# Optimization experiments

Measured on AMD Instinct MI355X. Metric: run time of the kernel, lower is better.

The kernel has to match this reference:

```python
import jax, jax.numpy as jnp
import numpy as np


def reference(x, phi, sigma, M_phi_plus, M_phi_minus, M_u, padded_sl):
    """STU forward: spectral FFT convolution + autoregressive input term.

    x:   (B, L, D) input sequence
    phi: (L, K) time-domain spectral filters (top-K Hankel eigenvectors);
         V = rfft(phi, n=padded_sl) matches the module's precomputed V.
    sigma: (K,) Hankel eigenvalues
    M_phi_plus/minus: (K, D, D) per-filter projections
    M_u: (k_u, D, D) AR-on-input matrices
    """
    B, L, D = x.shape
    K = sigma.shape[0]
    n = padded_sl  # FFT length for causal linear convolution

    # Alternating-sign trick for the 'minus' featurization:
    # sum_j (-1)^j phi_j u_{t-j} = (-1)^t * conv(phi, sgn*u)_t
    sgn = jnp.where(jnp.arange(L) % 2 == 0, 1.0, -1.0).astype(x.dtype)[None, :, None]  # (1,L,1)

    V = jnp.fft.rfft(phi, n=n, axis=0)                       # (n//2+1, K) complex
    U = jnp.fft.rfft(jnp.stack([x, x * sgn], axis=-1), n=n, axis=1)  # (B, n//2+1, D, 2)
    prod = V[None, :, :, None, None] * U[:, :, None, :, :]    # (B, n//2+1, K, D, 2)
    conv = jnp.fft.irfft(prod, n=n, axis=1)[:, :L]            # (B, L, K, D, 2) causal conv
    U_plus = conv[..., 0]
    U_minus = conv[..., 1] * sgn[..., None]                   # undo sign on output side

    # Fold sigma^{1/4} scaling into the projection matrices.
    sig4 = (sigma ** 0.25).astype(x.dtype)[:, None, None]     # (K,1,1)
    spectral = (
        jnp.einsum('blkd,kdo->blo', U_plus, M_phi_plus * sig4)
        + jnp.einsum('blkd,kdo->blo', U_minus, M_phi_minus * sig4)
    )

    # compute_ar_u: y_t += sum_{i=0}^{k_u-1} x_{t-i} @ M_u[i]  (use_ar_u=True)
    ar_u = jnp.einsum('bld,do->blo', x, M_u[0])
    for i in range(1, M_u.shape[0]):  # small fixed depth k_u=3
        x_shift = jnp.pad(x, ((0, 0), (i, 0), (0, 0)))[:, :L]
        ar_u = ar_u + jnp.einsum('bld,do->blo', x_shift, M_u[i])

    # use_ar_y=False branch; dropout=0 (identity)
    return spectral + ar_u


def setup_inputs() -> dict:
    key = jax.random.key(0)
    ks = jax.random.split(key, 6)
    B, L, D, K, KU, N = 1, 2048, 768, 16, 3, 4096
    x = jax.random.normal(ks[0], (B, L, D), jnp.float32)
    phi = jax.random.normal(ks[1], (L, K), jnp.float32) / np.sqrt(L).astype(np.float32)
    sigma = jax.random.uniform(ks[2], (K,), jnp.float32, 0.1, 1.0)
    M_phi_plus = jax.random.normal(ks[3], (K, D, D), jnp.float32) * 0.02
    M_phi_minus = jax.random.normal(ks[4], (K, D, D), jnp.float32) * 0.02
    M_u = jax.random.normal(ks[5], (KU, D, D), jnp.float32) * 0.02
    return {"x": x, "phi": phi, "sigma": sigma, "M_phi_plus": M_phi_plus,
            "M_phi_minus": M_phi_minus, "M_u": M_u, "padded_sl": N}
```

## Files before the change

### kernel.cpp

```cpp
#include <hip/hip_runtime.h>

typedef __attribute__((ext_vector_type(8))) short bf16x8;
typedef __attribute__((ext_vector_type(4))) float f32x4;

#define SL 2048
#define DM 768
#define NCH 32
#define MSPEC 24576
#define MTOT  26880

__device__ __forceinline__ short f2bf(float f) {
  unsigned u = __builtin_bit_cast(unsigned, f);
  u = (u + 0x7FFFu + ((u >> 16) & 1u)) >> 16;
  return (short)u;
}

__device__ __forceinline__ void gload16(const short* g, short* l) {
  __builtin_amdgcn_global_load_lds(
      (const __attribute__((address_space(1))) void*)g,
      (__attribute__((address_space(3))) void*)l, 16, 0, 0);
}


__global__ __launch_bounds__(256) void k_zero(float4* out) {
  out[blockIdx.x * 256 + threadIdx.x] = float4{0.f, 0.f, 0.f, 0.f};
}

__global__ __launch_bounds__(256) void k_prep_xT(const float* __restrict__ x,
                                                 short* __restrict__ xT) {
  __shared__ short tile[64][65];
  const int d0 = blockIdx.x * 64, l0 = blockIdx.y * 64;
  const int t = threadIdx.x;
#pragma unroll
  for (int rr = 0; rr < 16; ++rr) {
    int ll = rr * 4 + (t >> 6), dl = t & 63;
    tile[ll][dl] = f2bf(x[(size_t)(l0 + ll) * DM + d0 + dl]);
  }
  __syncthreads();
#pragma unroll
  for (int rr = 0; rr < 16; ++rr) {
    int dl = rr * 4 + (t >> 6), ll = t & 63;
    xT[(size_t)(d0 + dl) * SL + l0 + ll] = tile[ll][dl];
  }
}

__global__ __launch_bounds__(256) void k_prep_ar(const float* __restrict__ x,
                                                 short* __restrict__ U) {
  int id = blockIdx.x * 256 + threadIdx.x;
  int l = id / DM, d = id - l * DM;
#pragma unroll
  for (int i = 0; i < 3; ++i) {
    short v = 0;
    if (l >= i) v = f2bf(x[(size_t)(l - i) * DM + d]);
    U[(size_t)l * MTOT + MSPEC + i * DM + d] = v;
  }
}

__global__ __launch_bounds__(256) void k_prep_T(const float* __restrict__ phi,
                                                short* __restrict__ Tmat) {
  int idx = blockIdx.x * 256 + threadIdx.x;
  int b = idx & 127, a = (idx >> 7) & 127, dlag = (idx >> 14) & 15, c = idx >> 18;
  int j = dlag * 128 + a - b;
  short v = 0;
  if (j >= 0) {
    float p = phi[j * 16 + (c & 15)];
    if (c >= 16 && (j & 1)) p = -p;
    v = f2bf(p);
  }
  Tmat[idx] = v;
}

__global__ __launch_bounds__(256) void k_prep_M(const float* __restrict__ Mp,
                                                const float* __restrict__ Mm,
                                                const float* __restrict__ Mu,
                                                const float* __restrict__ sigma,
                                                short* __restrict__ McatT) {
  __shared__ short tile[64][65];
  const int m0 = blockIdx.x * 64, o0 = blockIdx.y * 64;
  const int t = threadIdx.x;
#pragma unroll
  for (int rr = 0; rr < 16; ++rr) {
    int ml = rr * 4 + (t >> 6), ol = t & 63;
    int m = m0 + ml, o = o0 + ol;
    float v;
    if (m < MSPEC) {
      int c = m / DM, d = m - c * DM;
      int k = c & 15;
      float s4 = sqrtf(sqrtf(sigma[k]));
      if (c < 16) v = Mp[((size_t)c * DM + d) * DM + o] * s4;
      else        v = Mm[((size_t)(c - 16) * DM + d) * DM + o] * s4;
    } else {
      int mm = m - MSPEC;
      int i = mm / DM, d = mm - i * DM;
      v = Mu[((size_t)i * DM + d) * DM + o];
    }
    tile[ml][ol] = f2bf(v);
  }
  __syncthreads();
#pragma unroll
  for (int rr = 0; rr < 16; ++rr) {
    int ol = rr * 4 + (t >> 6), ml = t & 63;
    McatT[(size_t)(o0 + ol) * MTOT + m0 + ml] = tile[ml][ol];
  }
}

__global__ __launch_bounds__(256) void k_gemm1(const short* __restrict__ Tmat,
                                               const short* __restrict__ xT,
                                               short* __restrict__ U) {
  __shared__ __align__(16) short As[2][128 * 32];
  __shared__ __align__(16) short Bs[2][128 * 32];
  const int wid = blockIdx.x;
  const int xcd = wid & 7;
  const int slot = wid >> 3;
  const int c = xcd * 4 + (slot & 3);
  const int dtile = (slot >> 2) % 6;
  const int ib = 15 - (slot >> 2) / 6;
  const int t = threadIdx.x;
  const int lane = t & 63, wave = t >> 6;
  const int wm = (wave >> 1) * 64, wn = (wave & 1) * 64;
  const int lrow = lane & 15, quad = lane >> 4;
  const int l4 = lane >> 2, lq = lane & 3;
  const int r0 = wave * 32 + l4;
  const int swz = (lq ^ ((l4 >> 1) & 3)) * 8;
  const int foff = ((quad ^ ((lrow >> 1) & 3)) << 3);

  f32x4 acc[4][4] = {};
  const short* Abase = Tmat + ((size_t)(c * 16) << 14) + r0 * 128 + swz;
  const short* Bbase = xT + (size_t)dtile * 128 * SL + (size_t)r0 * SL + swz;
  const int nit = 4 * (ib + 1);

  auto stage = [&](int it, int buf) {
    int dlag = it >> 2, kk = it & 3;
    const short* Ad = Abase + ((size_t)dlag << 14) + kk * 32;
    const short* Bd = Bbase + (ib - dlag) * 128 + kk * 32;
    short* lA = &As[buf][wave * 1024 + lane * 8];
    short* lB = &Bs[buf][wave * 1024 + lane * 8];
    gload16(Ad, lA);
    gload16(Ad + 16 * 128, lA + 512);
    gload16(Bd, lB);
    gload16(Bd + 16 * SL, lB + 512);
  };

  stage(0, 0);
  int cur = 0;
  for (int it = 0; it < nit; ++it) {
    __syncthreads();
    if (it + 1 < nit) stage(it + 1, cur ^ 1);
    bf16x8 af[4], bfr[4];
#pragma unroll
    for (int im = 0; im < 4; ++im)
      af[im] = *reinterpret_cast<const bf16x8*>(&As[cur][(wm + im * 16 + lrow) * 32 + foff]);
#pragma unroll
    for (int in = 0; in < 4; ++in)
      bfr[in] = *reinterpret_cast<const bf16x8*>(&Bs[cur][(wn + in * 16 + lrow) * 32 + foff]);
#pragma unroll
    for (int im = 0; im < 4; ++im)
#pragma unroll
      for (int in = 0; in < 4; ++in)
        acc[im][in] = __builtin_amdgcn_mfma_f32_16x16x32_bf16(af[im], bfr[in], acc[im][in], 0, 0, 0);
    cur ^= 1;
  }
  const int l0 = ib * 128, colbase = c * DM + dtile * 128;
#pragma unroll
  for (int im = 0; im < 4; ++im)
#pragma unroll
    for (int in = 0; in < 4; ++in)
#pragma unroll
      for (int r4 = 0; r4 < 4; ++r4) {
        int row = wm + im * 16 + quad * 4 + r4;
        int col = wn + in * 16 + lrow;
        U[(size_t)(l0 + row) * MTOT + colbase + col] = f2bf(acc[im][in][r4]);
      }
}

__global__ __launch_bounds__(256) void k_gemm2(const short* __restrict__ U,
                                               const short* __restrict__ McatT,
                                               float* __restrict__ out) {
  __shared__ __align__(16) short As[2][128 * 32];
  __shared__ __align__(16) short Bs[2][128 * 32];
  const int wid = blockIdx.x;
  const int kc = wid & 7;
  const int slot = wid >> 3;
  const int otile = slot % 6;
  const int lb = slot / 6;
  const int t = threadIdx.x;
  const int lane = t & 63, wave = t >> 6;
  const int wm = (wave >> 1) * 64, wn = (wave & 1) * 64;
  const int lrow = lane & 15, quad = lane >> 4;
  const int l4 = lane >> 2, lq = lane & 3;
  const int r0 = wave * 32 + l4;
  const int swz = (lq ^ ((l4 >> 1) & 3)) * 8;
  const int foff = ((quad ^ ((lrow >> 1) & 3)) << 3);

  f32x4 acc[4][4] = {};
  const short* Ab = U + (size_t)lb * 128 * MTOT + kc * 3360 + (size_t)r0 * MTOT + swz;
  const short* Bb = McatT + (size_t)otile * 128 * MTOT + kc * 3360 + (size_t)r0 * MTOT + swz;

  auto stage = [&](int s, int buf) {
    short* lA = &As[buf][wave * 1024 + lane * 8];
    short* lB = &Bs[buf][wave * 1024 + lane * 8];
    gload16(Ab + s * 32, lA);
    gload16(Ab + s * 32 + (size_t)16 * MTOT, lA + 512);
    gload16(Bb + s * 32, lB);
    gload16(Bb + s * 32 + (size_t)16 * MTOT, lB + 512);
  };

  stage(0, 0);
  int cur = 0;
  for (int s = 0; s < 105; ++s) {
    __syncthreads();
    if (s + 1 < 105) stage(s + 1, cur ^ 1);
    bf16x8 af[4], bfr[4];
#pragma unroll
    for (int im = 0; im < 4; ++im)
      af[im] = *reinterpret_cast<const bf16x8*>(&As[cur][(wm + im * 16 + lrow) * 32 + foff]);
#pragma unroll
    for (int in = 0; in < 4; ++in)
      bfr[in] = *reinterpret_cast<const bf16x8*>(&Bs[cur][(wn + in * 16 + lrow) * 32 + foff]);
#pragma unroll
    for (int im = 0; im < 4; ++im)
#pragma unroll
      for (int in = 0; in < 4; ++in)
        acc[im][in] = __builtin_amdgcn_mfma_f32_16x16x32_bf16(af[im], bfr[in], acc[im][in], 0, 0, 0);
    cur ^= 1;
  }
  const int l0 = lb * 128, o0 = otile * 128;
#pragma unroll
  for (int im = 0; im < 4; ++im)
#pragma unroll
    for (int in = 0; in < 4; ++in)
#pragma unroll
      for (int r4 = 0; r4 < 4; ++r4) {
        int row = wm + im * 16 + quad * 4 + r4;
        int col = wn + in * 16 + lrow;
        atomicAdd(&out[(size_t)(l0 + row) * DM + o0 + col], acc[im][in][r4]);
      }
}

extern "C" void kernel_launch(void* const* d_in, const int* in_sizes, int n_in,
                              void* d_out, int out_size, void* d_ws, size_t ws_size,
                              hipStream_t stream) {
  (void)in_sizes; (void)n_in; (void)out_size; (void)ws_size;
  const float* x     = (const float*)d_in[0];
  const float* phi   = (const float*)d_in[1];
  const float* sigma = (const float*)d_in[2];
  const float* Mp    = (const float*)d_in[3];
  const float* Mm    = (const float*)d_in[4];
  const float* Mu    = (const float*)d_in[5];
  float* out = (float*)d_out;
  char* ws = (char*)d_ws;

  short* U     = (short*)(ws);
  short* Tmat  = (short*)(ws + 110100480);
  short* xT    = (short*)(ws + 126877696);
  short* McatT = (short*)(ws + 130023424);

  k_zero<<<dim3(1536), dim3(256), 0, stream>>>((float4*)out);
  k_prep_xT<<<dim3(12, 32), dim3(256), 0, stream>>>(x, xT);
  k_prep_ar<<<dim3(6144), dim3(256), 0, stream>>>(x, U);
  k_prep_T<<<dim3(32768), dim3(256), 0, stream>>>(phi, Tmat);
  k_prep_M<<<dim3(420, 12), dim3(256), 0, stream>>>(Mp, Mm, Mu, sigma, McatT);
  k_gemm1<<<dim3(3072), dim3(256), 0, stream>>>(Tmat, xT, U);
  k_gemm2<<<dim3(768), dim3(256), 0, stream>>>(U, McatT, out);
}
```

Measured before the change: 416.9 us.

## Load MFMA fragments directly from global into registers with double buffering

Both GEMM kernels drop the LDS staging buffers, the async global-to-LDS copies and the per-step barriers. Each wave now loads its own bf16x8 MFMA fragments straight from global memory into registers, prefetching one k-step ahead with two register sets. The aim is to remove LDS traffic and synchronisation overhead. In exchange, waves that share rows no longer reuse tiles through LDS, so global and L2 traffic goes up. Each lane also reads only 16 bytes per row, which coalesces poorly.

```diff
diff --git a/kernel.cpp b/kernel.cpp
--- a/kernel.cpp
+++ b/kernel.cpp
@@ -13,12 +13,6 @@
   unsigned u = __builtin_bit_cast(unsigned, f);
   u = (u + 0x7FFFu + ((u >> 16) & 1u)) >> 16;
   return (short)u;
-}
-
-__device__ __forceinline__ void gload16(const short* g, short* l) {
-  __builtin_amdgcn_global_load_lds(
-      (const __attribute__((address_space(1))) void*)g,
-      (__attribute__((address_space(3))) void*)l, 16, 0, 0);
 }
 
 
@@ -107,59 +101,59 @@
 __global__ __launch_bounds__(256) void k_gemm1(const short* __restrict__ Tmat,
                                                const short* __restrict__ xT,
                                                short* __restrict__ U) {
-  __shared__ __align__(16) short As[2][128 * 32];
-  __shared__ __align__(16) short Bs[2][128 * 32];
   const int wid = blockIdx.x;
-  const int xcd = wid & 7;
   const int slot = wid >> 3;
-  const int c = xcd * 4 + (slot & 3);
+  const int c = (wid & 7) * 4 + (slot & 3);
   const int dtile = (slot >> 2) % 6;
   const int ib = 15 - (slot >> 2) / 6;
   const int t = threadIdx.x;
   const int lane = t & 63, wave = t >> 6;
   const int wm = (wave >> 1) * 64, wn = (wave & 1) * 64;
   const int lrow = lane & 15, quad = lane >> 4;
-  const int l4 = lane >> 2, lq = lane & 3;
-  const int r0 = wave * 32 + l4;
-  const int swz = (lq ^ ((l4 >> 1) & 3)) * 8;
-  const int foff = ((quad ^ ((lrow >> 1) & 3)) << 3);
+
+  const short* aRow[4];
+  const short* bRow[4];
+#pragma unroll
+  for (int im = 0; im < 4; ++im)
+    aRow[im] = Tmat + (((size_t)c * 16) << 14) + (wm + im * 16 + lrow) * 128 + quad * 8;
+#pragma unroll
+  for (int in = 0; in < 4; ++in)
+    bRow[in] = xT + (size_t)(dtile * 128 + wn + in * 16 + lrow) * SL + quad * 8;
 
   f32x4 acc[4][4] = {};
-  const short* Abase = Tmat + ((size_t)(c * 16) << 14) + r0 * 128 + swz;
-  const short* Bbase = xT + (size_t)dtile * 128 * SL + (size_t)r0 * SL + swz;
+  bf16x8 a0[4], b0[4], a1[4], b1[4];
   const int nit = 4 * (ib + 1);
 
-  auto stage = [&](int it, int buf) {
-    int dlag = it >> 2, kk = it & 3;
-    const short* Ad = Abase + ((size_t)dlag << 14) + kk * 32;
-    const short* Bd = Bbase + (ib - dlag) * 128 + kk * 32;
-    short* lA = &As[buf][wave * 1024 + lane * 8];
-    short* lB = &Bs[buf][wave * 1024 + lane * 8];
-    gload16(Ad, lA);
-    gload16(Ad + 16 * 128, lA + 512);
-    gload16(Bd, lB);
-    gload16(Bd + 16 * SL, lB + 512);
-  };
-
-  stage(0, 0);
-  int cur = 0;
-  for (int it = 0; it < nit; ++it) {
-    __syncthreads();
-    if (it + 1 < nit) stage(it + 1, cur ^ 1);
-    bf16x8 af[4], bfr[4];
-#pragma unroll
-    for (int im = 0; im < 4; ++im)
-      af[im] = *reinterpret_cast<const bf16x8*>(&As[cur][(wm + im * 16 + lrow) * 32 + foff]);
-#pragma unroll
-    for (int in = 0; in < 4; ++in)
-      bfr[in] = *reinterpret_cast<const bf16x8*>(&Bs[cur][(wn + in * 16 + lrow) * 32 + foff]);
+  auto ld = [&](int it, bf16x8* A, bf16x8* B) {
+    const int dlag = it >> 2, kk = it & 3;
+    const int aOff = dlag * (128 * 128) + kk * 32;
+    const int bOff = (ib - dlag) * 128 + kk * 32;
+#pragma unroll
+    for (int im = 0; im < 4; ++im)
+      A[im] = *reinterpret_cast<const bf16x8*>(aRow[im] + aOff);
+#pragma unroll
+    for (int in = 0; in < 4; ++in)
+      B[in] = *reinterpret_cast<const bf16x8*>(bRow[in] + bOff);
+  };
+  auto mm = [&](bf16x8* A, bf16x8* B) {
 #pragma unroll
     for (int im = 0; im < 4; ++im)
 #pragma unroll
       for (int in = 0; in < 4; ++in)
-        acc[im][in] = __builtin_amdgcn_mfma_f32_16x16x32_bf16(af[im], bfr[in], acc[im][in], 0, 0, 0);
-    cur ^= 1;
-  }
+        acc[im][in] = __builtin_amdgcn_mfma_f32_16x16x32_bf16(A[im], B[in], acc[im][in], 0, 0, 0);
+  };
+
+  ld(0, a0, b0);
+  ld(1, a1, b1);
+  for (int it = 0; it < nit - 2; it += 2) {
+    mm(a0, b0);
+    ld(it + 2, a0, b0);
+    mm(a1, b1);
+    if (it + 3 < nit) ld(it + 3, a1, b1);
+  }
+  mm(a0, b0);
+  mm(a1, b1);
+
   const int l0 = ib * 128, colbase = c * DM + dtile * 128;
 #pragma unroll
   for (int im = 0; im < 4; ++im)
@@ -176,54 +170,57 @@
 __global__ __launch_bounds__(256) void k_gemm2(const short* __restrict__ U,
                                                const short* __restrict__ McatT,
                                                float* __restrict__ out) {
-  __shared__ __align__(16) short As[2][128 * 32];
-  __shared__ __align__(16) short Bs[2][128 * 32];
   const int wid = blockIdx.x;
   const int kc = wid & 7;
   const int slot = wid >> 3;
   const int otile = slot % 6;
   const int lb = slot / 6;
+  const int ns = 105;
   const int t = threadIdx.x;
   const int lane = t & 63, wave = t >> 6;
   const int wm = (wave >> 1) * 64, wn = (wave & 1) * 64;
   const int lrow = lane & 15, quad = lane >> 4;
-  const int l4 = lane >> 2, lq = lane & 3;
-  const int r0 = wave * 32 + l4;
-  const int swz = (lq ^ ((l4 >> 1) & 3)) * 8;
-  const int foff = ((quad ^ ((lrow >> 1) & 3)) << 3);
+
+  const short* aRow[4];
+  const short* bRow[4];
+#pragma unroll
+  for (int im = 0; im < 4; ++im)
+    aRow[im] = U + (size_t)(lb * 128 + wm + im * 16 + lrow) * MTOT + kc * 3360 + quad * 8;
+#pragma unroll
+  for (int in = 0; in < 4; ++in)
+    bRow[in] = McatT + (size_t)(otile * 128 + wn + in * 16 + lrow) * MTOT + kc * 3360 + quad * 8;
 
   f32x4 acc[4][4] = {};
-  const short* Ab = U + (size_t)lb * 128 * MTOT + kc * 3360 + (size_t)r0 * MTOT + swz;
-  const short* Bb = McatT + (size_t)otile * 128 * MTOT + kc * 3360 + (size_t)r0 * MTOT + swz;
-
-  auto stage = [&](int s, int buf) {
-    short* lA = &As[buf][wave * 1024 + lane * 8];
-    short* lB = &Bs[buf][wave * 1024 + lane * 8];
-    gload16(Ab + s * 32, lA);
-    gload16(Ab + s * 32 + (size_t)16 * MTOT, lA + 512);
-    gload16(Bb + s * 32, lB);
-    gload16(Bb + s * 32 + (size_t)16 * MTOT, lB + 512);
-  };
-
-  stage(0, 0);
-  int cur = 0;
-  for (int s = 0; s < 105; ++s) {
-    __syncthreads();
-    if (s + 1 < 105) stage(s + 1, cur ^ 1);
-    bf16x8 af[4], bfr[4];
-#pragma unroll
-    for (int im = 0; im < 4; ++im)
-      af[im] = *reinterpret_cast<const bf16x8*>(&As[cur][(wm + im * 16 + lrow) * 32 + foff]);
-#pragma unroll
-    for (int in = 0; in < 4; ++in)
-      bfr[in] = *reinterpret_cast<const bf16x8*>(&Bs[cur][(wn + in * 16 + lrow) * 32 + foff]);
+  bf16x8 a0[4], b0[4], a1[4], b1[4];
+
+  auto ld = [&](int s, bf16x8* A, bf16x8* B) {
+    const int off = s * 32;
+#pragma unroll
+    for (int im = 0; im < 4; ++im)
+      A[im] = *reinterpret_cast<const bf16x8*>(aRow[im] + off);
+#pragma unroll
+    for (int in = 0; in < 4; ++in)
+      B[in] = *reinterpret_cast<const bf16x8*>(bRow[in] + off);
+  };
+  auto mm = [&](bf16x8* A, bf16x8* B) {
 #pragma unroll
     for (int im = 0; im < 4; ++im)
 #pragma unroll
       for (int in = 0; in < 4; ++in)
-        acc[im][in] = __builtin_amdgcn_mfma_f32_16x16x32_bf16(af[im], bfr[in], acc[im][in], 0, 0, 0);
-    cur ^= 1;
-  }
+        acc[im][in] = __builtin_amdgcn_mfma_f32_16x16x32_bf16(A[im], B[in], acc[im][in], 0, 0, 0);
+  };
+
+  ld(0, a0, b0);
+  ld(1, a1, b1);
+  for (int s = 0; s < ns - 2; s += 2) {
+    mm(a0, b0);
+    ld(s + 2, a0, b0);
+    mm(a1, b1);
+    if (s + 3 < ns) ld(s + 3, a1, b1);
+  }
+  mm(a0, b0);
+  if ((ns & 1) == 0) mm(a1, b1);
+
   const int l0 = lb * 128, o0 = otile * 128;
 #pragma unroll
   for (int im = 0; im < 4; ++im)
```

Result: slower. 842.7 us (+102.2%).

## Merge prep kernels into front kernel and overlap M transpose with GEMM1

Applied to the files above, without the earlier changes.

Merges the zero, x-transpose, Toeplitz-build and AR-prep kernels into one launch selected by block index. Moves the M projection transpose into the same launch as the first GEMM so it runs alongside those GEMM blocks. Vectorises the Toeplitz and AR prep to write 8 bf16 values per thread with 16-byte stores. This cuts launch count and lets memory-bound prep overlap compute-bound GEMM work, at the cost of heterogeneous blocks sharing one launch's resource limits.

```diff
diff --git a/kernel.cpp b/kernel.cpp
--- a/kernel.cpp
+++ b/kernel.cpp
@@ -5,7 +5,6 @@
 
 #define SL 2048
 #define DM 768
-#define NCH 32
 #define MSPEC 24576
 #define MTOT  26880
 
@@ -21,156 +20,173 @@
       (__attribute__((address_space(3))) void*)l, 16, 0, 0);
 }
 
-
-__global__ __launch_bounds__(256) void k_zero(float4* out) {
-  out[blockIdx.x * 256 + threadIdx.x] = float4{0.f, 0.f, 0.f, 0.f};
-}
-
-__global__ __launch_bounds__(256) void k_prep_xT(const float* __restrict__ x,
-                                                 short* __restrict__ xT) {
-  __shared__ short tile[64][65];
-  const int d0 = blockIdx.x * 64, l0 = blockIdx.y * 64;
+__global__ __launch_bounds__(256) void k_front(const float* __restrict__ x,
+                                               const float* __restrict__ phi,
+                                               float* __restrict__ out,
+                                               short* __restrict__ xT,
+                                               short* __restrict__ Tmat,
+                                               short* __restrict__ U) {
+  __shared__ short tile[64 * 65];
+  const int wid = blockIdx.x;
   const int t = threadIdx.x;
-#pragma unroll
-  for (int rr = 0; rr < 16; ++rr) {
-    int ll = rr * 4 + (t >> 6), dl = t & 63;
-    tile[ll][dl] = f2bf(x[(size_t)(l0 + ll) * DM + d0 + dl]);
+
+  if (wid < 1536) {
+    reinterpret_cast<float4*>(out)[(size_t)wid * 256 + t] = float4{0.f, 0.f, 0.f, 0.f};
+
+  } else if (wid < 1920) {
+    const int b = wid - 1536;
+    const int d0 = (b % 12) * 64, l0 = (b / 12) * 64;
+#pragma unroll
+    for (int rr = 0; rr < 16; ++rr) {
+      int ll = rr * 4 + (t >> 6), dl = t & 63;
+      tile[ll * 65 + dl] = f2bf(x[(size_t)(l0 + ll) * DM + d0 + dl]);
+    }
+    __syncthreads();
+#pragma unroll
+    for (int rr = 0; rr < 16; ++rr) {
+      int dl = rr * 4 + (t >> 6), ll = t & 63;
+      xT[(size_t)(d0 + dl) * SL + l0 + ll] = tile[ll * 65 + dl];
+    }
+
+  } else if (wid < 6016) {
+    int g = (wid - 1920) * 256 + t;
+    int b8 = g & 15, a = (g >> 4) & 127, dlag = (g >> 11) & 15, c = g >> 15;
+    int k = c & 15;
+    int jb = dlag * 128 + a - b8 * 8;
+    short v[8];
+#pragma unroll
+    for (int i2 = 0; i2 < 8; ++i2) {
+      int j = jb - i2;
+      float p = 0.f;
+      if (j >= 0) {
+        p = phi[j * 16 + k];
+        if (c >= 16 && (j & 1)) p = -p;
+      }
+      v[i2] = f2bf(p);
+    }
+    *reinterpret_cast<int4*>(Tmat + (size_t)g * 8) = *reinterpret_cast<const int4*>(v);
+
+  } else {
+    int g = (wid - 6016) * 256 + t;
+    int d8 = g % 96;
+    int rest = g / 96;
+    int l = rest & 2047, i = rest >> 11;
+    int d = d8 * 8;
+    short v[8] = {0, 0, 0, 0, 0, 0, 0, 0};
+    if (l >= i) {
+      const float4* src = reinterpret_cast<const float4*>(x + (size_t)(l - i) * DM + d);
+      float4 f0 = src[0], f1 = src[1];
+      v[0] = f2bf(f0.x); v[1] = f2bf(f0.y); v[2] = f2bf(f0.z); v[3] = f2bf(f0.w);
+      v[4] = f2bf(f1.x); v[5] = f2bf(f1.y); v[6] = f2bf(f1.z); v[7] = f2bf(f1.w);
+    }
+    *reinterpret_cast<int4*>(U + (size_t)l * MTOT + MSPEC + i * DM + d) =
+        *reinterpret_cast<const int4*>(v);
   }
-  __syncthreads();
-#pragma unroll
-  for (int rr = 0; rr < 16; ++rr) {
-    int dl = rr * 4 + (t >> 6), ll = t & 63;
-    xT[(size_t)(d0 + dl) * SL + l0 + ll] = tile[ll][dl];
-  }
-}
-
-__global__ __launch_bounds__(256) void k_prep_ar(const float* __restrict__ x,
-                                                 short* __restrict__ U) {
-  int id = blockIdx.x * 256 + threadIdx.x;
-  int l = id / DM, d = id - l * DM;
-#pragma unroll
-  for (int i = 0; i < 3; ++i) {
-    short v = 0;
-    if (l >= i) v = f2bf(x[(size_t)(l - i) * DM + d]);
-    U[(size_t)l * MTOT + MSPEC + i * DM + d] = v;
-  }
-}
-
-__global__ __launch_bounds__(256) void k_prep_T(const float* __restrict__ phi,
-                                                short* __restrict__ Tmat) {
-  int idx = blockIdx.x * 256 + threadIdx.x;
-  int b = idx & 127, a = (idx >> 7) & 127, dlag = (idx >> 14) & 15, c = idx >> 18;
-  int j = dlag * 128 + a - b;
-  short v = 0;
-  if (j >= 0) {
-    float p = phi[j * 16 + (c & 15)];
-    if (c >= 16 && (j & 1)) p = -p;
-    v = f2bf(p);
-  }
-  Tmat[idx] = v;
-}
-
-__global__ __launch_bounds__(256) void k_prep_M(const float* __restrict__ Mp,
-                                                const float* __restrict__ Mm,
-                                                const float* __restrict__ Mu,
-                                                const float* __restrict__ sigma,
-                                                short* __restrict__ McatT) {
-  __shared__ short tile[64][65];
-  const int m0 = blockIdx.x * 64, o0 = blockIdx.y * 64;
-  const int t = threadIdx.x;
-#pragma unroll
-  for (int rr = 0; rr < 16; ++rr) {
-    int ml = rr * 4 + (t >> 6), ol = t & 63;
-    int m = m0 + ml, o = o0 + ol;
-    float v;
-    if (m < MSPEC) {
-      int c = m / DM, d = m - c * DM;
-      int k = c & 15;
-      float s4 = sqrtf(sqrtf(sigma[k]));
-      if (c < 16) v = Mp[((size_t)c * DM + d) * DM + o] * s4;
-      else        v = Mm[((size_t)(c - 16) * DM + d) * DM + o] * s4;
-    } else {
-      int mm = m - MSPEC;
-      int i = mm / DM, d = mm - i * DM;
-      v = Mu[((size_t)i * DM + d) * DM + o];
-    }
-    tile[ml][ol] = f2bf(v);
-  }
-  __syncthreads();
-#pragma unroll
-  for (int rr = 0; rr < 16; ++rr) {
-    int ol = rr * 4 + (t >> 6), ml = t & 63;
-    McatT[(size_t)(o0 + ol) * MTOT + m0 + ml] = tile[ml][ol];
-  }
-}
-
-__global__ __launch_bounds__(256) void k_gemm1(const short* __restrict__ Tmat,
-                                               const short* __restrict__ xT,
-                                               short* __restrict__ U) {
+}
+
+__global__ __launch_bounds__(256) void k_mid(const short* __restrict__ Tmat,
+                                             const short* __restrict__ xT,
+                                             short* __restrict__ U,
+                                             const float* __restrict__ Mp,
+                                             const float* __restrict__ Mm,
+                                             const float* __restrict__ Mu,
+                                             const float* __restrict__ sigma,
+                                             short* __restrict__ McatT) {
   __shared__ __align__(16) short As[2][128 * 32];
   __shared__ __align__(16) short Bs[2][128 * 32];
   const int wid = blockIdx.x;
-  const int xcd = wid & 7;
-  const int slot = wid >> 3;
-  const int c = xcd * 4 + (slot & 3);
-  const int dtile = (slot >> 2) % 6;
-  const int ib = 15 - (slot >> 2) / 6;
   const int t = threadIdx.x;
-  const int lane = t & 63, wave = t >> 6;
-  const int wm = (wave >> 1) * 64, wn = (wave & 1) * 64;
-  const int lrow = lane & 15, quad = lane >> 4;
-  const int l4 = lane >> 2, lq = lane & 3;
-  const int r0 = wave * 32 + l4;
-  const int swz = (lq ^ ((l4 >> 1) & 3)) * 8;
-  const int foff = ((quad ^ ((lrow >> 1) & 3)) << 3);
-
-  f32x4 acc[4][4] = {};
-  const short* Abase = Tmat + ((size_t)(c * 16) << 14) + r0 * 128 + swz;
-  const short* Bbase = xT + (size_t)dtile * 128 * SL + (size_t)r0 * SL + swz;
-  const int nit = 4 * (ib + 1);
-
-  auto stage = [&](int it, int buf) {
-    int dlag = it >> 2, kk = it & 3;
-    const short* Ad = Abase + ((size_t)dlag << 14) + kk * 32;
-    const short* Bd = Bbase + (ib - dlag) * 128 + kk * 32;
-    short* lA = &As[buf][wave * 1024 + lane * 8];
-    short* lB = &Bs[buf][wave * 1024 + lane * 8];
-    gload16(Ad, lA);
-    gload16(Ad + 16 * 128, lA + 512);
-    gload16(Bd, lB);
-    gload16(Bd + 16 * SL, lB + 512);
-  };
-
-  stage(0, 0);
-  int cur = 0;
-  for (int it = 0; it < nit; ++it) {
+
+  if (wid < 3072) {
+    const int slot = wid >> 3;
+    const int c = (wid & 7) * 4 + (slot & 3);
+    const int dtile = (slot >> 2) % 6;
+    const int ib = 15 - (slot >> 2) / 6;
+    const int lane = t & 63, wave = t >> 6;
+    const int wm = (wave >> 1) * 64, wn = (wave & 1) * 64;
+    const int lrow = lane & 15, quad = lane >> 4;
+    const int l4 = lane >> 2, lq = lane & 3;
+    const int r0 = wave * 32 + l4;
+    const int swz = (lq ^ ((l4 >> 1) & 3)) * 8;
+    const int foff = ((quad ^ ((lrow >> 1) & 3)) << 3);
+
+    f32x4 acc[4][4] = {};
+    const short* Abase = Tmat + (((size_t)c * 16) << 14) + r0 * 128 + swz;
+    const short* Bbase = xT + (size_t)dtile * 128 * SL + (size_t)r0 * SL + swz;
+    const int nit = 4 * (ib + 1);
+
+    auto stage = [&](int it, int buf) {
+      int dlag = it >> 2, kk = it & 3;
+      const short* Ad = Abase + ((size_t)dlag << 14) + kk * 32;
+      const short* Bd = Bbase + (ib - dlag) * 128 + kk * 32;
+      short* lA = &As[buf][wave * 1024 + lane * 8];
+      short* lB = &Bs[buf][wave * 1024 + lane * 8];
+      gload16(Ad, lA);
+      gload16(Ad + 16 * 128, lA + 512);
+      gload16(Bd, lB);
+      gload16(Bd + 16 * SL, lB + 512);
+    };
+
+    stage(0, 0);
+    int cur = 0;
+    for (int it = 0; it < nit; ++it) {
+      __syncthreads();
+      if (it + 1 < nit) stage(it + 1, cur ^ 1);
+      bf16x8 af[4], bfr[4];
+#pragma unroll
+      for (int im = 0; im < 4; ++im)
+        af[im] = *reinterpret_cast<const bf16x8*>(&As[cur][(wm + im * 16 + lrow) * 32 + foff]);
+#pragma unroll
+      for (int in = 0; in < 4; ++in)
+        bfr[in] = *reinterpret_cast<const bf16x8*>(&Bs[cur][(wn + in * 16 + lrow) * 32 + foff]);
+#pragma unroll
+      for (int im = 0; im < 4; ++im)
+#pragma unroll
+        for (int in = 0; in < 4; ++in)
+          acc[im][in] = __builtin_amdgcn_mfma_f32_16x16x32_bf16(af[im], bfr[in], acc[im][in], 0, 0, 0);
+      cur ^= 1;
+    }
+    const int l0 = ib * 128, colbase = c * DM + dtile * 128;
+#pragma unroll
+    for (int im = 0; im < 4; ++im)
+#pragma unroll
+      for (int in = 0; in < 4; ++in)
+#pragma unroll
+        for (int r4 = 0; r4 < 4; ++r4) {
+          int row = wm + im * 16 + quad * 4 + r4;
+          int col = wn + in * 16 + lrow;
+          U[(size_t)(l0 + row) * MTOT + colbase + col] = f2bf(acc[im][in][r4]);
+        }
+
+  } else {
+    short* tile = &As[0][0];
+    const int idx = wid - 3072;
+    const int m0 = (idx % 420) * 64, o0 = (idx / 420) * 64;
+#pragma unroll
+    for (int rr = 0; rr < 16; ++rr) {
+      int ml = rr * 4 + (t >> 6), ol = t & 63;
+      int m = m0 + ml, o = o0 + ol;
+      float v;
+      if (m < MSPEC) {
+        int c = m / DM, d = m - c * DM;
+        int k = c & 15;
+        float s4 = sqrtf(sqrtf(sigma[k]));
+        if (c < 16) v = Mp[((size_t)c * DM + d) * DM + o] * s4;
+        else        v = Mm[((size_t)(c - 16) * DM + d) * DM + o] * s4;
+      } else {
+        int mm = m - MSPEC;
+        int i = mm / DM, d = mm - i * DM;
+        v = Mu[((size_t)i * DM + d) * DM + o];
+      }
+      tile[ml * 65 + ol] = f2bf(v);
+    }
     __syncthreads();
-    if (it + 1 < nit) stage(it + 1, cur ^ 1);
-    bf16x8 af[4], bfr[4];
-#pragma unroll
-    for (int im = 0; im < 4; ++im)
-      af[im] = *reinterpret_cast<const bf16x8*>(&As[cur][(wm + im * 16 + lrow) * 32 + foff]);
-#pragma unroll
-    for (int in = 0; in < 4; ++in)
-      bfr[in] = *reinterpret_cast<const bf16x8*>(&Bs[cur][(wn + in * 16 + lrow) * 32 + foff]);
-#pragma unroll
-    for (int im = 0; im < 4; ++im)
-#pragma unroll
-      for (int in = 0; in < 4; ++in)
-        acc[im][in] = __builtin_amdgcn_mfma_f32_16x16x32_bf16(af[im], bfr[in], acc[im][in], 0, 0, 0);
-    cur ^= 1;
+#pragma unroll
+    for (int rr = 0; rr < 16; ++rr) {
+      int ol = rr * 4 + (t >> 6), ml = t & 63;
+      McatT[(size_t)(o0 + ol) * MTOT + m0 + ml] = tile[ml * 65 + ol];
+    }
   }
-  const int l0 = ib * 128, colbase = c * DM + dtile * 128;
-#pragma unroll
-  for (int im = 0; im < 4; ++im)
-#pragma unroll
-    for (int in = 0; in < 4; ++in)
-#pragma unroll
-      for (int r4 = 0; r4 < 4; ++r4) {
-        int row = wm + im * 16 + quad * 4 + r4;
-        int col = wn + in * 16 + lrow;
-        U[(size_t)(l0 + row) * MTOT + colbase + col] = f2bf(acc[im][in][r4]);
-      }
 }
 
 __global__ __launch_bounds__(256) void k_gemm2(const short* __restrict__ U,
@@ -255,11 +271,7 @@
   short* xT    = (short*)(ws + 126877696);
   short* McatT = (short*)(ws + 130023424);
 
-  k_zero<<<dim3(1536), dim3(256), 0, stream>>>((float4*)out);
-  k_prep_xT<<<dim3(12, 32), dim3(256), 0, stream>>>(x, xT);
-  k_prep_ar<<<dim3(6144), dim3(256), 0, stream>>>(x, U);
-  k_prep_T<<<dim3(32768), dim3(256), 0, stream>>>(phi, Tmat);
-  k_prep_M<<<dim3(420, 12), dim3(256), 0, stream>>>(Mp, Mm, Mu, sigma, McatT);
-  k_gemm1<<<dim3(3072), dim3(256), 0, stream>>>(Tmat, xT, U);
+  k_front<<<dim3(8320), dim3(256), 0, stream>>>(x, phi, out, xT, Tmat, U);
+  k_mid<<<dim3(8112), dim3(256), 0, stream>>>(Tmat, xT, U, Mp, Mm, Mu, sigma, McatT);
   k_gemm2<<<dim3(768), dim3(256), 0, stream>>>(U, McatT, out);
 }
```

Measured after the change: 444.2 us. 1.07x slower.
